# Optimization experiments

Hardware: AMD Instinct MI355X
Metric: run time of the kernel (lower is better)

The kernel has to match this reference:

```python
import jax, jax.numpy as jnp
import numpy as np
from functools import partial

NX, NY = 48, 48
LX, LY = 1.0, 1.0
T, DT = 0.01, 0.0001
NT = int(T / DT)  # 100 sequential explicit-Euler steps
DX, DY = LX / NX, LY / NY
TWO_PI = 2.0 * jnp.pi


def setup_inputs() -> dict:
    key = jax.random.key(0)
    u0 = jax.random.normal(key, (8192, 1, NX, NY), dtype=jnp.float32)
    return {
        "u0": u0,
        "alpha_w1": jnp.float32(0.1),
        "alpha_w2": jnp.float32(0.1),
        "alpha_w3": jnp.float32(0.1),
        "beta_w1": jnp.float32(0.3),
        "beta_w2": jnp.float32(0.2),
        "beta_w3": jnp.float32(0.1),
    }


def _coeff_grids(a1, a2, a3, b1, b2, b3):
    x = jnp.linspace(0.0, LX, NX)
    y = jnp.linspace(0.0, LY, NY)
    yy, xx = jnp.meshgrid(y, x, indexing="ij")  # (NY, NX), matches torch.meshgrid(y, x, 'ij')
    alpha = 0.5 * DT * (jnp.abs(a1) + jnp.abs(a2) * jnp.sin(TWO_PI * yy)
                        + jnp.abs(a3) * jnp.cos(TWO_PI * yy)) / DX ** 2
    beta = DT * (jnp.abs(b1) + jnp.abs(b2) * jnp.cos(TWO_PI * xx)
                 + jnp.abs(b3) * jnp.sin(TWO_PI * xx)) / DY ** 2
    return alpha[None], beta[None]  # (1, NY, NX) broadcast over batch (square grid)


def reference(u0, alpha_w1, alpha_w2, alpha_w3, beta_w1, beta_w2, beta_w3):
    alpha_grid, beta_grid = _coeff_grids(alpha_w1, alpha_w2, alpha_w3,
                                         beta_w1, beta_w2, beta_w3)
    u = u0[:, 0]  # (B, NX, NY)
    # reflect-pad once; the boundary ring stays frozen across all timesteps
    u = jnp.pad(u, ((0, 0), (1, 1), (1, 1)), mode="reflect")

    def step(u, _):
        ui = u[:, 1:-1, 1:-1]
        u_xx = u[:, 2:, 1:-1] - 2.0 * ui + u[:, :-2, 1:-1]
        u_yy = u[:, 1:-1, 2:] - 2.0 * ui + u[:, 1:-1, :-2]
        u = u.at[:, 1:-1, 1:-1].set(ui + alpha_grid * u_xx + beta_grid * u_yy)
        return u, None

    u, _ = jax.lax.scan(step, u, None, length=NT)
    return u[:, 1:-1, 1:-1][:, None]  # (B, 1, NX, NY)
```

## Files before the change

### kernel.cpp

```cpp
#include <hip/hip_runtime.h>
#include <hip/hip_fp16.h>
#include <math.h>


#define NTSTEPS 100

typedef __half2 h2;

__device__ __forceinline__ h2 dpp_row_shr1(h2 oldv, h2 x) {
    int r = __builtin_amdgcn_update_dpp(
        __builtin_bit_cast(int, oldv), __builtin_bit_cast(int, x),
        0x111, 0xF, 0xF, false);
    return __builtin_bit_cast(h2, r);
}
__device__ __forceinline__ h2 dpp_row_shl1(h2 oldv, h2 x) {
    int r = __builtin_amdgcn_update_dpp(
        __builtin_bit_cast(int, oldv), __builtin_bit_cast(int, x),
        0x101, 0xF, 0xF, false);
    return __builtin_bit_cast(h2, r);
}
__device__ __forceinline__ h2 bperm(int addr, h2 x) {
    int r = __builtin_amdgcn_ds_bpermute(addr, __builtin_bit_cast(int, x));
    return __builtin_bit_cast(h2, r);
}

__global__ __launch_bounds__(256, 4) void pde_kernel(
    const float* __restrict__ u0,
    const float* __restrict__ pa1, const float* __restrict__ pa2,
    const float* __restrict__ pa3, const float* __restrict__ pb1,
    const float* __restrict__ pb2, const float* __restrict__ pb3,
    float* __restrict__ out)
{
    __shared__ float sh_a[48];
    __shared__ float sh_b[48];

    const int tid  = threadIdx.x;
    const int lane = tid & 63;
    const int wv   = tid >> 6;
    const int pair = blockIdx.x * 4 + wv;
    const int tx   = lane & 15;
    const int ty   = lane >> 4;
    const int c0   = 3 * tx;
    const int r0   = 12 * ty;

    if (tid < 48) {
        float a1 = fabsf(pa1[0]), a2 = fabsf(pa2[0]), a3 = fabsf(pa3[0]);
        float b1 = fabsf(pb1[0]), b2 = fabsf(pb2[0]), b3 = fabsf(pb3[0]);
        float t = 6.283185307179586f * ((float)tid / 47.0f);
        float s = sinf(t), c = cosf(t);
        sh_a[tid] = 0.1152f * (a1 + a2 * s + a3 * c);
        sh_b[tid] = 0.2304f * (b1 + b2 * c + b3 * s);
    }
    __syncthreads();

    const float* __restrict__ srcA = u0 + (size_t)(2 * pair) * 2304;
    const float* __restrict__ srcB = srcA + 2304;

    h2 a[12], b[3];
    #pragma unroll
    for (int k = 0; k < 12; ++k) a[k] = __half2half2(__float2half(sh_a[r0 + k]));
    #pragma unroll
    for (int c = 0; c < 3; ++c) b[c] = __half2half2(__float2half(sh_b[c0 + c]));
    const h2 neg2 = __floats2half2_rn(-2.0f, -2.0f);

    h2 u[12][3];
    h2 ep[12];
    h2 tH[3], bH[3];

    const int epc = (tx == 15) ? 46 : 1;
    #pragma unroll
    for (int k = 0; k < 12; ++k) {
        #pragma unroll
        for (int c = 0; c < 3; ++c) {
            int o = (r0 + k) * 48 + c0 + c;
            u[k][c] = __floats2half2_rn(srcA[o], srcB[o]);
        }
        int oe = (r0 + k) * 48 + epc;
        ep[k] = __floats2half2_rn(srcA[oe], srcB[oe]);
    }
    {
        const int tor = (ty == 0) ? 1 : (r0 - 1);
        const int bor = (ty == 3) ? 46 : (r0 + 12);
        #pragma unroll
        for (int c = 0; c < 3; ++c) {
            int ot = tor * 48 + c0 + c, ob = bor * 48 + c0 + c;
            tH[c] = __floats2half2_rn(srcA[ot], srcB[ot]);
            bH[c] = __floats2half2_rn(srcA[ob], srcB[ob]);
        }
    }

    const int upA = ((lane - 16) & 63) << 2;
    const int dnA = ((lane + 16) & 63) << 2;
    const bool notTop = (ty != 0);
    const bool notBot = (ty != 3);

    #pragma unroll 1
    for (int t = 0; t < NTSTEPS; ++t) {
        #pragma unroll
        for (int c = 0; c < 3; ++c) {
            h2 tv = bperm(upA, u[11][c]);
            h2 bv = bperm(dnA, u[0][c]);
            tH[c] = notTop ? tv : tH[c];
            bH[c] = notBot ? bv : bH[c];
        }
        h2 p0 = tH[0], p1 = tH[1], p2 = tH[2];
        #pragma unroll
        for (int k = 0; k < 12; ++k) {
            const h2 x0 = u[k][0], x1 = u[k][1], x2 = u[k][2];
            const h2 hl = dpp_row_shr1(ep[k], x2);
            const h2 hr = dpp_row_shl1(ep[k], x0);
            const h2 d0 = (k == 11) ? bH[0] : u[k + 1][0];
            const h2 d1 = (k == 11) ? bH[1] : u[k + 1][1];
            const h2 d2 = (k == 11) ? bH[2] : u[k + 1][2];
            const h2 s10 = __hadd2(p0, d0);
            const h2 s11 = __hadd2(p1, d1);
            const h2 s12 = __hadd2(p2, d2);
            const h2 s20 = __hadd2(hl, x1);
            const h2 s21 = __hadd2(x0, x2);
            const h2 s22 = __hadd2(x1, hr);
            const h2 t10 = __hfma2(neg2, x0, s10);
            const h2 t11 = __hfma2(neg2, x1, s11);
            const h2 t12 = __hfma2(neg2, x2, s12);
            const h2 t20 = __hfma2(neg2, x0, s20);
            const h2 t21 = __hfma2(neg2, x1, s21);
            const h2 t22 = __hfma2(neg2, x2, s22);
            const h2 n0 = __hfma2(b[0], t20, __hfma2(a[k], t10, x0));
            const h2 n1 = __hfma2(b[1], t21, __hfma2(a[k], t11, x1));
            const h2 n2 = __hfma2(b[2], t22, __hfma2(a[k], t12, x2));
            p0 = x0; p1 = x1; p2 = x2;
            u[k][0] = n0; u[k][1] = n1; u[k][2] = n2;
        }
    }

    float* __restrict__ dstA = out + (size_t)(2 * pair) * 2304;
    float* __restrict__ dstB = dstA + 2304;
    #pragma unroll
    for (int k = 0; k < 12; ++k) {
        #pragma unroll
        for (int c = 0; c < 3; ++c) {
            int o = (r0 + k) * 48 + c0 + c;
            dstA[o] = __low2float(u[k][c]);
            dstB[o] = __high2float(u[k][c]);
        }
    }
}

extern "C" void kernel_launch(void* const* d_in, const int* in_sizes, int n_in,
                              void* d_out, int out_size, void* d_ws, size_t ws_size,
                              hipStream_t stream) {
    const float* u0 = (const float*)d_in[0];
    pde_kernel<<<1024, 256, 0, stream>>>(
        u0,
        (const float*)d_in[1], (const float*)d_in[2], (const float*)d_in[3],
        (const float*)d_in[4], (const float*)d_in[5], (const float*)d_in[6],
        (float*)d_out);
}
```

Baseline: 349.2 us.

## Pack mirrored rows of one image into half2 instead of two images per wave

```diff
diff --git a/kernel.cpp b/kernel.cpp
--- a/kernel.cpp
+++ b/kernel.cpp
@@ -23,124 +23,139 @@
     int r = __builtin_amdgcn_ds_bpermute(addr, __builtin_bit_cast(int, x));
     return __builtin_bit_cast(h2, r);
 }
+__device__ __forceinline__ h2 swap16(h2 x) {
+    unsigned int v = __builtin_bit_cast(unsigned int, x);
+    return __builtin_bit_cast(h2, (v >> 16) | (v << 16));
+}
 
-__global__ __launch_bounds__(256, 4) void pde_kernel(
+__global__ __launch_bounds__(256, 8) void pde_kernel(
     const float* __restrict__ u0,
     const float* __restrict__ pa1, const float* __restrict__ pa2,
     const float* __restrict__ pa3, const float* __restrict__ pb1,
     const float* __restrict__ pb2, const float* __restrict__ pb3,
     float* __restrict__ out)
 {
-    __shared__ float sh_a[48];
-    __shared__ float sh_b[48];
-
     const int tid  = threadIdx.x;
     const int lane = tid & 63;
     const int wv   = tid >> 6;
-    const int pair = blockIdx.x * 4 + wv;
+    const int img  = blockIdx.x * 4 + wv;
     const int tx   = lane & 15;
     const int ty   = lane >> 4;
     const int c0   = 3 * tx;
-    const int r0   = 12 * ty;
+    const int rlo0 = 6 * ty;
 
-    if (tid < 48) {
-        float a1 = fabsf(pa1[0]), a2 = fabsf(pa2[0]), a3 = fabsf(pa3[0]);
-        float b1 = fabsf(pb1[0]), b2 = fabsf(pb2[0]), b3 = fabsf(pb3[0]);
-        float t = 6.283185307179586f * ((float)tid / 47.0f);
-        float s = sinf(t), c = cosf(t);
-        sh_a[tid] = 0.1152f * (a1 + a2 * s + a3 * c);
-        sh_b[tid] = 0.2304f * (b1 + b2 * c + b3 * s);
+    const float a1 = fabsf(pa1[0]), a2 = fabsf(pa2[0]), a3 = fabsf(pa3[0]);
+    const float b1 = fabsf(pb1[0]), b2 = fabsf(pb2[0]), b3 = fabsf(pb3[0]);
+    const float C = 6.283185307179586f / 47.0f;
+    h2 a[6], b[3];
+    #pragma unroll
+    for (int k = 0; k < 6; ++k) {
+        int rl = rlo0 + k, rh = 47 - rl;
+        float alo = 0.1152f * (a1 + a2 * sinf(C * rl) + a3 * cosf(C * rl));
+        float ahi = 0.1152f * (a1 + a2 * sinf(C * rh) + a3 * cosf(C * rh));
+        a[k] = __floats2half2_rn(alo, ahi);
     }
-    __syncthreads();
-
-    const float* __restrict__ srcA = u0 + (size_t)(2 * pair) * 2304;
-    const float* __restrict__ srcB = srcA + 2304;
-
-    h2 a[12], b[3];
     #pragma unroll
-    for (int k = 0; k < 12; ++k) a[k] = __half2half2(__float2half(sh_a[r0 + k]));
-    #pragma unroll
-    for (int c = 0; c < 3; ++c) b[c] = __half2half2(__float2half(sh_b[c0 + c]));
+    for (int c = 0; c < 3; ++c) {
+        int col = c0 + c;
+        float bb = 0.2304f * (b1 + b2 * cosf(C * col) + b3 * sinf(C * col));
+        b[c] = __half2half2(__float2half(bb));
+    }
     const h2 neg2 = __floats2half2_rn(-2.0f, -2.0f);
 
-    h2 u[12][3];
-    h2 ep[12];
-    h2 tH[3], bH[3];
+    const float* __restrict__ src = u0 + (size_t)img * 2304;
+    h2 u[6][3];
+    h2 ep[6];
+    h2 padV[3];
 
     const int epc = (tx == 15) ? 46 : 1;
     #pragma unroll
-    for (int k = 0; k < 12; ++k) {
+    for (int k = 0; k < 6; ++k) {
+        int rl = rlo0 + k, rh = 47 - rl;
         #pragma unroll
-        for (int c = 0; c < 3; ++c) {
-            int o = (r0 + k) * 48 + c0 + c;
-            u[k][c] = __floats2half2_rn(srcA[o], srcB[o]);
+        for (int c = 0; c < 3; ++c)
+            u[k][c] = __floats2half2_rn(src[rl * 48 + c0 + c],
+                                        src[rh * 48 + c0 + c]);
+        ep[k] = __floats2half2_rn(src[rl * 48 + epc], src[rh * 48 + epc]);
+    }
+    #pragma unroll
+    for (int c = 0; c < 3; ++c)
+        padV[c] = __floats2half2_rn(src[48 + c0 + c], src[46 * 48 + c0 + c]);
+
+    const int upA = ((lane - 16) & 63) << 2;
+    const int dnA = ((lane + 16) & 63) << 2;
+    const bool top = (ty == 0);
+    const bool bot = (ty == 3);
+
+    #pragma unroll 1
+    for (int t = 0; t < NTSTEPS; ++t) {
+        h2 wT0 = bperm(upA, u[5][0]);
+        h2 wT1 = bperm(upA, u[5][1]);
+        h2 wT2 = bperm(upA, u[5][2]);
+        h2 wB0 = bperm(dnA, u[0][0]);
+        h2 wB1 = bperm(dnA, u[0][1]);
+        h2 wB2 = bperm(dnA, u[0][2]);
+
+        h2 o1_0 = u[1][0], o1_1 = u[1][1], o1_2 = u[1][2];
+        h2 p0 = u[0][0], p1 = u[0][1], p2 = u[0][2];
+
+        #pragma unroll
+        for (int k = 1; k <= 4; ++k) {
+            const h2 x0 = u[k][0], x1 = u[k][1], x2 = u[k][2];
+            const h2 hl = dpp_row_shr1(ep[k], x2);
+            const h2 hr = dpp_row_shl1(ep[k], x0);
+            const h2 d0 = u[k + 1][0], d1 = u[k + 1][1], d2 = u[k + 1][2];
+            const h2 v0 = __hadd2(p0, d0), v1 = __hadd2(p1, d1), v2 = __hadd2(p2, d2);
+            const h2 g0 = __hadd2(hl, x1), g1 = __hadd2(x0, x2), g2 = __hadd2(x1, hr);
+            const h2 t10 = __hfma2(neg2, x0, v0), t11 = __hfma2(neg2, x1, v1), t12 = __hfma2(neg2, x2, v2);
+            const h2 t20 = __hfma2(neg2, x0, g0), t21 = __hfma2(neg2, x1, g1), t22 = __hfma2(neg2, x2, g2);
+            u[k][0] = __hfma2(b[0], t20, __hfma2(a[k], t10, x0));
+            u[k][1] = __hfma2(b[1], t21, __hfma2(a[k], t11, x1));
+            u[k][2] = __hfma2(b[2], t22, __hfma2(a[k], t12, x2));
+            p0 = x0; p1 = x1; p2 = x2;
         }
-        int oe = (r0 + k) * 48 + epc;
-        ep[k] = __floats2half2_rn(srcA[oe], srcB[oe]);
-    }
-    {
-        const int tor = (ty == 0) ? 1 : (r0 - 1);
-        const int bor = (ty == 3) ? 46 : (r0 + 12);
-        #pragma unroll
-        for (int c = 0; c < 3; ++c) {
-            int ot = tor * 48 + c0 + c, ob = bor * 48 + c0 + c;
-            tH[c] = __floats2half2_rn(srcA[ot], srcB[ot]);
-            bH[c] = __floats2half2_rn(srcA[ob], srcB[ob]);
+
+        {
+            const h2 x0 = u[5][0], x1 = u[5][1], x2 = u[5][2];
+            const h2 bh0 = bot ? swap16(x0) : wB0;
+            const h2 bh1 = bot ? swap16(x1) : wB1;
+            const h2 bh2 = bot ? swap16(x2) : wB2;
+            const h2 hl = dpp_row_shr1(ep[5], x2);
+            const h2 hr = dpp_row_shl1(ep[5], x0);
+            const h2 v0 = __hadd2(p0, bh0), v1 = __hadd2(p1, bh1), v2 = __hadd2(p2, bh2);
+            const h2 g0 = __hadd2(hl, x1), g1 = __hadd2(x0, x2), g2 = __hadd2(x1, hr);
+            const h2 t10 = __hfma2(neg2, x0, v0), t11 = __hfma2(neg2, x1, v1), t12 = __hfma2(neg2, x2, v2);
+            const h2 t20 = __hfma2(neg2, x0, g0), t21 = __hfma2(neg2, x1, g1), t22 = __hfma2(neg2, x2, g2);
+            u[5][0] = __hfma2(b[0], t20, __hfma2(a[5], t10, x0));
+            u[5][1] = __hfma2(b[1], t21, __hfma2(a[5], t11, x1));
+            u[5][2] = __hfma2(b[2], t22, __hfma2(a[5], t12, x2));
+        }
+
+        {
+            const h2 x0 = u[0][0], x1 = u[0][1], x2 = u[0][2];
+            const h2 th0 = top ? padV[0] : wT0;
+            const h2 th1 = top ? padV[1] : wT1;
+            const h2 th2 = top ? padV[2] : wT2;
+            const h2 hl = dpp_row_shr1(ep[0], x2);
+            const h2 hr = dpp_row_shl1(ep[0], x0);
+            const h2 v0 = __hadd2(th0, o1_0), v1 = __hadd2(th1, o1_1), v2 = __hadd2(th2, o1_2);
+            const h2 g0 = __hadd2(hl, x1), g1 = __hadd2(x0, x2), g2 = __hadd2(x1, hr);
+            const h2 t10 = __hfma2(neg2, x0, v0), t11 = __hfma2(neg2, x1, v1), t12 = __hfma2(neg2, x2, v2);
+            const h2 t20 = __hfma2(neg2, x0, g0), t21 = __hfma2(neg2, x1, g1), t22 = __hfma2(neg2, x2, g2);
+            u[0][0] = __hfma2(b[0], t20, __hfma2(a[0], t10, x0));
+            u[0][1] = __hfma2(b[1], t21, __hfma2(a[0], t11, x1));
+            u[0][2] = __hfma2(b[2], t22, __hfma2(a[0], t12, x2));
         }
     }
 
-    const int upA = ((lane - 16) & 63) << 2;
-    const int dnA = ((lane + 16) & 63) << 2;
-    const bool notTop = (ty != 0);
-    const bool notBot = (ty != 3);
-
-    #pragma unroll 1
-    for (int t = 0; t < NTSTEPS; ++t) {
+    float* __restrict__ dst = out + (size_t)img * 2304;
+    #pragma unroll
+    for (int k = 0; k < 6; ++k) {
+        int rl = rlo0 + k, rh = 47 - rl;
         #pragma unroll
         for (int c = 0; c < 3; ++c) {
-            h2 tv = bperm(upA, u[11][c]);
-            h2 bv = bperm(dnA, u[0][c]);
-            tH[c] = notTop ? tv : tH[c];
-            bH[c] = notBot ? bv : bH[c];
-        }
-        h2 p0 = tH[0], p1 = tH[1], p2 = tH[2];
-        #pragma unroll
-        for (int k = 0; k < 12; ++k) {
-            const h2 x0 = u[k][0], x1 = u[k][1], x2 = u[k][2];
-            const h2 hl = dpp_row_shr1(ep[k], x2);
-            const h2 hr = dpp_row_shl1(ep[k], x0);
-            const h2 d0 = (k == 11) ? bH[0] : u[k + 1][0];
-            const h2 d1 = (k == 11) ? bH[1] : u[k + 1][1];
-            const h2 d2 = (k == 11) ? bH[2] : u[k + 1][2];
-            const h2 s10 = __hadd2(p0, d0);
-            const h2 s11 = __hadd2(p1, d1);
-            const h2 s12 = __hadd2(p2, d2);
-            const h2 s20 = __hadd2(hl, x1);
-            const h2 s21 = __hadd2(x0, x2);
-            const h2 s22 = __hadd2(x1, hr);
-            const h2 t10 = __hfma2(neg2, x0, s10);
-            const h2 t11 = __hfma2(neg2, x1, s11);
-            const h2 t12 = __hfma2(neg2, x2, s12);
-            const h2 t20 = __hfma2(neg2, x0, s20);
-            const h2 t21 = __hfma2(neg2, x1, s21);
-            const h2 t22 = __hfma2(neg2, x2, s22);
-            const h2 n0 = __hfma2(b[0], t20, __hfma2(a[k], t10, x0));
-            const h2 n1 = __hfma2(b[1], t21, __hfma2(a[k], t11, x1));
-            const h2 n2 = __hfma2(b[2], t22, __hfma2(a[k], t12, x2));
-            p0 = x0; p1 = x1; p2 = x2;
-            u[k][0] = n0; u[k][1] = n1; u[k][2] = n2;
-        }
-    }
-
-    float* __restrict__ dstA = out + (size_t)(2 * pair) * 2304;
-    float* __restrict__ dstB = dstA + 2304;
-    #pragma unroll
-    for (int k = 0; k < 12; ++k) {
-        #pragma unroll
-        for (int c = 0; c < 3; ++c) {
-            int o = (r0 + k) * 48 + c0 + c;
-            dstA[o] = __low2float(u[k][c]);
-            dstB[o] = __high2float(u[k][c]);
+            dst[rl * 48 + c0 + c] = __low2float(u[k][c]);
+            dst[rh * 48 + c0 + c] = __high2float(u[k][c]);
         }
     }
 }
@@ -149,7 +164,7 @@
                               void* d_out, int out_size, void* d_ws, size_t ws_size,
                               hipStream_t stream) {
     const float* u0 = (const float*)d_in[0];
-    pde_kernel<<<1024, 256, 0, stream>>>(
+    pde_kernel<<<2048, 256, 0, stream>>>(
         u0,
         (const float*)d_in[1], (const float*)d_in[2], (const float*)d_in[3],
         (const float*)d_in[4], (const float*)d_in[5], (const float*)d_in[6],
```

Result: slower. 370.1 us (+6.0%).
